# Optimization experiments

Measured on AMD Instinct MI355X. Metric: run time of the kernel, lower is better.

## Reference

```python
import jax, jax.numpy as jnp
import numpy as np

B, C, T, Fd = 4, 256, 64, 256
H = 8
HID = int(C * 2.0)
LN_EPS = 1e-5
L2_EPS = 1e-12


def _layernorm(x, g, b):
    mu = jnp.mean(x, axis=-1, keepdims=True)
    var = jnp.mean((x - mu) ** 2, axis=-1, keepdims=True)
    return (x - mu) * jax.lax.rsqrt(var + LN_EPS) * g + b


def _l2norm(x):
    n = jnp.sqrt(jnp.sum(x * x, axis=-1, keepdims=True))
    return x / jnp.maximum(n, L2_EPS)


def setup_inputs() -> dict:
    key = jax.random.key(0)
    ks = jax.random.split(key, 8)
    s = 0.02
    return {
        "x": jax.random.normal(ks[0], (B, C, T, Fd), dtype=jnp.float32),
        "norm1_g": jnp.ones((C,), jnp.float32),
        "norm1_b": jnp.zeros((C,), jnp.float32),
        "Wqkv": jax.random.normal(ks[1], (C, 3 * C), jnp.float32) * s,
        "dw_w": jax.random.normal(ks[2], (3 * C, 1, 3), jnp.float32) * s,  # depthwise conv1d kernel (O, I/g=1, K)
        "Wproj": jax.random.normal(ks[3], (C, C), jnp.float32) * s,
        "temperature": jnp.full((H, 1, 1), 0.5, jnp.float32),
        "norm2_g": jnp.ones((C,), jnp.float32),
        "norm2_b": jnp.zeros((C,), jnp.float32),
        "W1": jax.random.normal(ks[4], (C, HID), jnp.float32) * s,
        "b1": jnp.zeros((HID,), jnp.float32),
        "W2": jax.random.normal(ks[5], (HID, C), jnp.float32) * s,
        "b2": jnp.zeros((C,), jnp.float32),
    }


def reference(x, norm1_g, norm1_b, Wqkv, dw_w, Wproj, temperature,
              norm2_g, norm2_b, W1, b1, W2, b2):
    b, c, t, f = x.shape
    # axis='freq': (b c t f) -> ((b t) f c)
    xs = jnp.transpose(x, (0, 2, 3, 1)).reshape(b * t, f, c)

    xn = _layernorm(xs, norm1_g, norm1_b)
    qkv = xn @ Wqkv                                  # (bt, f, 3c)
    # depthwise conv1d along the sequence (freq) axis, kernel 3, pad 1
    qkv = jnp.transpose(qkv, (0, 2, 1))              # (bt, 3c, f)
    qkv = jax.lax.conv_general_dilated(
        qkv, dw_w, window_strides=(1,), padding=[(1, 1)],
        feature_group_count=3 * c,
        dimension_numbers=("NCH", "OIH", "NCH"))
    qkv = jnp.transpose(qkv, (0, 2, 1))              # (bt, f, 3c)

    q, k, v = jnp.split(qkv, 3, axis=-1)
    d = c // H
    def heads(z):  # (bt, s, c) -> (bt, h, s, d)
        return jnp.transpose(z.reshape(b * t, f, H, d), (0, 2, 1, 3))
    q, k, v = heads(q), heads(k), heads(v)

    q = _l2norm(q)
    k = _l2norm(k)
    attn = jnp.einsum("bhsd,bhtd->bhst", q, k) * temperature  # temp broadcasts (h,1,1)
    attn = jax.nn.softmax(attn, axis=-1)
    out = jnp.einsum("bhst,bhtd->bhsd", attn, v)
    out = jnp.transpose(out, (0, 2, 1, 3)).reshape(b * t, f, c)
    out = out @ Wproj
    out = out + xs

    h = _layernorm(out, norm2_g, norm2_b)
    h = jax.nn.gelu(h @ W1 + b1, approximate=False) @ W2 + b2
    out = out + h

    # ((b t) f c) -> (b c t f)
    out = out.reshape(b, t, f, c)
    return jnp.transpose(out, (0, 3, 1, 2))
```

## Files before the change

### kernel.cpp

```cpp
#include <hip/hip_runtime.h>
#include <math.h>

#define Bv 4
#define Cv 256
#define Tv 64
#define Fv 256
#define Hv 8
#define HIDv 512
#define Mv 65536
#define CTF (Cv * Tv * Fv)
#define TF (Tv * Fv)

typedef unsigned short u16;
typedef __attribute__((ext_vector_type(8))) short bfx8;
typedef __attribute__((ext_vector_type(4))) float f32x4;

__device__ __forceinline__ float bf2f(u16 u) {
  return __uint_as_float(((unsigned int)u) << 16);
}
__device__ __forceinline__ u16 f2bf(float f) {
  unsigned int x = __float_as_uint(f);
  unsigned int r = x + 0x7fffu + ((x >> 16) & 1u);
  return (u16)(r >> 16);
}

__launch_bounds__(256)
__global__ void transpose_w(const float* __restrict__ in, u16* __restrict__ out,
                            int K, int N) {
  __shared__ float t[32][33];
  const int n0 = blockIdx.x * 32, k0 = blockIdx.y * 32;
  const int c = threadIdx.x & 31, r = threadIdx.x >> 5;
#pragma unroll
  for (int i = 0; i < 4; ++i)
    t[r + 8 * i][c] = in[(size_t)(k0 + r + 8 * i) * N + n0 + c];
  __syncthreads();
#pragma unroll
  for (int i = 0; i < 4; ++i)
    out[(size_t)(n0 + r + 8 * i) * K + k0 + c] = f2bf(t[c][r + 8 * i]);
}

__launch_bounds__(256)
__global__ void ln1_kernel(const float* __restrict__ x, const float* __restrict__ g,
                           const float* __restrict__ bta, u16* __restrict__ xn) {
  __shared__ float tile[256][33];
  __shared__ float red1[8][32];
  __shared__ float red2[8][32];
  __shared__ float mu_s[32];
  __shared__ float rs_s[32];
  const int tid = threadIdx.x;
  const int blk = blockIdx.x;
  const int n = blk >> 3;
  const int f0 = (blk & 7) << 5;
  const int bb = n >> 6, tt = n & 63;
  const float* xb = x + (size_t)bb * CTF + (size_t)tt * Fv;
  const int fl = tid & 31, c0 = tid >> 5;
#pragma unroll
  for (int i = 0; i < 32; ++i) {
    int c = i * 8 + c0;
    tile[c][fl] = xb[(size_t)c * TF + f0 + fl];
  }
  __syncthreads();
  const int col = tid & 31, part = tid >> 5;
  float s = 0.f, s2 = 0.f;
#pragma unroll
  for (int i = 0; i < 32; ++i) {
    float v = tile[part * 32 + i][col];
    s += v; s2 += v * v;
  }
  red1[part][col] = s; red2[part][col] = s2;
  __syncthreads();
  if (tid < 32) {
    float S1 = 0.f, S2 = 0.f;
#pragma unroll
    for (int p = 0; p < 8; ++p) { S1 += red1[p][tid]; S2 += red2[p][tid]; }
    float m = S1 * (1.f / 256.f);
    float var = S2 * (1.f / 256.f) - m * m;
    mu_s[tid] = m;
    rs_s[tid] = rsqrtf(var + 1e-5f);
  }
  __syncthreads();
  const float gv = g[tid], bv = bta[tid];
  u16* ob = xn + ((size_t)n * 256 + f0) * 256 + tid;
#pragma unroll
  for (int fl2 = 0; fl2 < 32; ++fl2) {
    ob[(size_t)fl2 * 256] = f2bf((tile[tid][fl2] - mu_s[fl2]) * rs_s[fl2] * gv + bv);
  }
}

template <int K, int N, int EPI>
__launch_bounds__(256)
__global__ void gemm_mfma(const u16* __restrict__ A, const u16* __restrict__ Bt,
                          void* __restrict__ Cc, const float* __restrict__ aux0,
                          const u16* __restrict__ aux1) {
  constexpr int LDSTR = 88;
  __shared__ u16 As[128 * LDSTR];
  __shared__ u16 Bs[128 * LDSTR];
  const int tid = threadIdx.x;
  const int lane = tid & 63, wid = tid >> 6;
  const int m0 = blockIdx.y * 128, n0 = blockIdx.x * 128;
  const int wm = (wid & 1) * 64, wn = (wid >> 1) * 64;
  const int lm = lane & 15, quad = lane >> 4;

  const int srow = tid >> 3, sch = tid & 7;

  f32x4 acc[4][4] = {};
  for (int k0 = 0; k0 < K; k0 += 64) {
    bfx8 ar[4], br[4];
#pragma unroll
    for (int i = 0; i < 4; ++i) {
      const int row = srow + i * 32;
      ar[i] = *(const bfx8*)(A + (size_t)(m0 + row) * K + k0 + sch * 8);
      br[i] = *(const bfx8*)(Bt + (size_t)(n0 + row) * K + k0 + sch * 8);
    }
    __syncthreads();
#pragma unroll
    for (int i = 0; i < 4; ++i) {
      const int row = srow + i * 32;
      *(bfx8*)&As[row * LDSTR + sch * 8] = ar[i];
      *(bfx8*)&Bs[row * LDSTR + sch * 8] = br[i];
    }
    __syncthreads();
#pragma unroll
    for (int s = 0; s < 2; ++s) {
      bfx8 af[4], bf[4];
#pragma unroll
      for (int t = 0; t < 4; ++t) {
        af[t] = *(const bfx8*)&As[(wm + t * 16 + lm) * LDSTR + s * 32 + quad * 8];
        bf[t] = *(const bfx8*)&Bs[(wn + t * 16 + lm) * LDSTR + s * 32 + quad * 8];
      }
#pragma unroll
      for (int tm = 0; tm < 4; ++tm)
#pragma unroll
        for (int tn = 0; tn < 4; ++tn)
          acc[tm][tn] = __builtin_amdgcn_mfma_f32_16x16x32_bf16(af[tm], bf[tn], acc[tm][tn], 0, 0, 0);
    }
  }

  const int row_l = quad * 4;
  const int nn = m0 >> 8;
  const int bb = nn >> 6, tt = nn & 63;
  const int srow_base = (m0 & 255) + wm;
  float bcol[4];
  if constexpr (EPI == 2 || EPI == 3) {
#pragma unroll
    for (int tn = 0; tn < 4; ++tn) bcol[tn] = aux0[n0 + wn + tn * 16 + lm];
  }
#pragma unroll
  for (int tm = 0; tm < 4; ++tm) {
    const int grow0 = m0 + wm + tm * 16 + row_l;
    const int sr0 = srow_base + tm * 16 + row_l;
#pragma unroll
    for (int tn = 0; tn < 4; ++tn) {
      const int gcol = n0 + wn + tn * 16 + lm;
      if constexpr (EPI == 0) {
#pragma unroll
        for (int r = 0; r < 4; ++r)
          ((u16*)Cc)[(size_t)(grow0 + r) * N + gcol] = f2bf(acc[tm][tn][r]);
      } else if constexpr (EPI == 1) {
        const float4 xv = *(const float4*)(aux0 + (size_t)bb * CTF + (size_t)gcol * TF + tt * Fv + sr0);
        const float xr[4] = {xv.x, xv.y, xv.z, xv.w};
#pragma unroll
        for (int r = 0; r < 4; ++r)
          ((u16*)Cc)[(size_t)(grow0 + r) * N + gcol] = f2bf(acc[tm][tn][r] + xr[r]);
      } else if constexpr (EPI == 2) {
#pragma unroll
        for (int r = 0; r < 4; ++r) {
          float v = acc[tm][tn][r] + bcol[tn];
          float y = 0.79788456080286536f * (v + 0.044715f * v * v * v);
          float th = 1.f - 2.f / (__expf(2.f * y) + 1.f);
          ((u16*)Cc)[(size_t)(grow0 + r) * N + gcol] = f2bf(0.5f * v * (1.f + th));
        }
      } else {
        float4 o;
#pragma unroll
        for (int r = 0; r < 4; ++r) {
          float res = bf2f(aux1[(size_t)(grow0 + r) * 256 + gcol]);
          ((float*)&o)[r] = acc[tm][tn][r] + bcol[tn] + res;
        }
        *(float4*)((float*)Cc + (size_t)bb * CTF + (size_t)gcol * TF + tt * Fv + sr0) = o;
      }
    }
  }
}

__launch_bounds__(256)
__global__ void attn_kernel(const u16* __restrict__ qkv, const float* __restrict__ dw,
                            const float* __restrict__ temp, u16* __restrict__ attn_out) {
  __shared__ u16 Qs[256 * 40];
  __shared__ u16 Kc[64 * 40];
  __shared__ u16 Vtc[32 * 72];
  __shared__ u16 Pw[4 * 64 * 72];
  __shared__ float l_s[256];
  const int tid = threadIdx.x;
  const int lane = tid & 63, w = tid >> 6;
  const int l15 = lane & 15, quad = lane >> 4;
  const int n = blockIdx.x >> 3, h = blockIdx.x & 7;
  const int h32 = h * 32;
  const u16* base = qkv + (size_t)n * 256 * 768;
  const float th = temp[h];

  const int dg = tid & 3, d0 = dg * 8;
  const int rloc = tid >> 2;

  float wtsK[3][8], wtsV[3][8];
#pragma unroll
  for (int j = 0; j < 8; ++j) {
    const int chk = 256 + h32 + d0 + j;
    const int chv = 512 + h32 + d0 + j;
#pragma unroll
    for (int t = 0; t < 3; ++t) {
      wtsK[t][j] = dw[chk * 3 + t];
      wtsV[t][j] = dw[chv * 3 + t];
    }
  }

  {
    float wtsQ[3][8];
#pragma unroll
    for (int j = 0; j < 8; ++j)
#pragma unroll
      for (int t = 0; t < 3; ++t) wtsQ[t][j] = dw[(h32 + d0 + j) * 3 + t];
#pragma unroll
    for (int p = 0; p < 4; ++p) {
      const int row = p * 64 + rloc;
      const u16* src = base + (size_t)row * 768 + h32 + d0;
      float v[8];
      const bfx8 bmid = *(const bfx8*)src;
#pragma unroll
      for (int j = 0; j < 8; ++j) v[j] = wtsQ[1][j] * bf2f((u16)bmid[j]);
      if (row > 0) {
        const bfx8 bprv = *(const bfx8*)(src - 768);
#pragma unroll
        for (int j = 0; j < 8; ++j) v[j] += wtsQ[0][j] * bf2f((u16)bprv[j]);
      }
      if (row < 255) {
        const bfx8 bnxt = *(const bfx8*)(src + 768);
#pragma unroll
        for (int j = 0; j < 8; ++j) v[j] += wtsQ[2][j] * bf2f((u16)bnxt[j]);
      }
      float ssq = 0.f;
#pragma unroll
      for (int j = 0; j < 8; ++j) ssq += v[j] * v[j];
      ssq += __shfl_xor(ssq, 1);
      ssq += __shfl_xor(ssq, 2);
      const float inv = 1.f / fmaxf(sqrtf(ssq), 1e-12f);
      bfx8 qb;
#pragma unroll
      for (int j = 0; j < 8; ++j) qb[j] = (short)f2bf(v[j] * inv);
      *(bfx8*)&Qs[row * 40 + d0] = qb;
    }
  }
  __syncthreads();

  bfx8 bq[4];
#pragma unroll
  for (int ct = 0; ct < 4; ++ct)
    bq[ct] = *(const bfx8*)&Qs[(w * 64 + ct * 16 + l15) * 40 + quad * 8];

  u16* PwB = Pw + w * (64 * 72);
  const f32x4 zf = {0.f, 0.f, 0.f, 0.f};
  f32x4 acc[4][2] = {};
  float lsum[4] = {0.f, 0.f, 0.f, 0.f};

  for (int c = 0; c < 4; ++c) {
    {
      const int grow = c * 64 + rloc;
      const u16* srcK = base + (size_t)grow * 768 + 256 + h32 + d0;
      float v[8];
      const bfx8 bmid = *(const bfx8*)srcK;
#pragma unroll
      for (int j = 0; j < 8; ++j) v[j] = wtsK[1][j] * bf2f((u16)bmid[j]);
      if (grow > 0) {
        const bfx8 bprv = *(const bfx8*)(srcK - 768);
#pragma unroll
        for (int j = 0; j < 8; ++j) v[j] += wtsK[0][j] * bf2f((u16)bprv[j]);
      }
      if (grow < 255) {
        const bfx8 bnxt = *(const bfx8*)(srcK + 768);
#pragma unroll
        for (int j = 0; j < 8; ++j) v[j] += wtsK[2][j] * bf2f((u16)bnxt[j]);
      }
      float ssq = 0.f;
#pragma unroll
      for (int j = 0; j < 8; ++j) ssq += v[j] * v[j];
      ssq += __shfl_xor(ssq, 1);
      ssq += __shfl_xor(ssq, 2);
      const float inv = 1.f / fmaxf(sqrtf(ssq), 1e-12f);
      bfx8 kb;
#pragma unroll
      for (int j = 0; j < 8; ++j) kb[j] = (short)f2bf(v[j] * inv);
      *(bfx8*)&Kc[rloc * 40 + d0] = kb;

      const u16* srcV = base + (size_t)grow * 768 + 512 + h32 + d0;
      float vv[8];
      const bfx8 vmid = *(const bfx8*)srcV;
#pragma unroll
      for (int j = 0; j < 8; ++j) vv[j] = wtsV[1][j] * bf2f((u16)vmid[j]);
      if (grow > 0) {
        const bfx8 vprv = *(const bfx8*)(srcV - 768);
#pragma unroll
        for (int j = 0; j < 8; ++j) vv[j] += wtsV[0][j] * bf2f((u16)vprv[j]);
      }
      if (grow < 255) {
        const bfx8 vnxt = *(const bfx8*)(srcV + 768);
#pragma unroll
        for (int j = 0; j < 8; ++j) vv[j] += wtsV[2][j] * bf2f((u16)vnxt[j]);
      }
#pragma unroll
      for (int j = 0; j < 8; ++j) Vtc[(d0 + j) * 72 + rloc] = f2bf(vv[j]);
    }
    __syncthreads();

#pragma unroll
    for (int rt = 0; rt < 4; ++rt) {
      const bfx8 af = *(const bfx8*)&Kc[(rt * 16 + l15) * 40 + quad * 8];
#pragma unroll
      for (int ct = 0; ct < 4; ++ct) {
        f32x4 sc = __builtin_amdgcn_mfma_f32_16x16x32_bf16(af, bq[ct], zf, 0, 0, 0);
        float e0 = __expf(sc[0] * th);
        float e1 = __expf(sc[1] * th);
        float e2 = __expf(sc[2] * th);
        float e3 = __expf(sc[3] * th);
        lsum[ct] += (e0 + e1) + (e2 + e3);
        uint2 pk;
        pk.x = (unsigned int)f2bf(e0) | ((unsigned int)f2bf(e1) << 16);
        pk.y = (unsigned int)f2bf(e2) | ((unsigned int)f2bf(e3) << 16);
        *(uint2*)&PwB[(ct * 16 + l15) * 72 + rt * 16 + quad * 4] = pk;
      }
    }

#pragma unroll
    for (int ks = 0; ks < 2; ++ks) {
      const bfx8 bv0 = *(const bfx8*)&Vtc[l15 * 72 + ks * 32 + quad * 8];
      const bfx8 bv1 = *(const bfx8*)&Vtc[(16 + l15) * 72 + ks * 32 + quad * 8];
#pragma unroll
      for (int rt2 = 0; rt2 < 4; ++rt2) {
        const bfx8 ap = *(const bfx8*)&PwB[(rt2 * 16 + l15) * 72 + ks * 32 + quad * 8];
        acc[rt2][0] = __builtin_amdgcn_mfma_f32_16x16x32_bf16(ap, bv0, acc[rt2][0], 0, 0, 0);
        acc[rt2][1] = __builtin_amdgcn_mfma_f32_16x16x32_bf16(ap, bv1, acc[rt2][1], 0, 0, 0);
      }
    }
    __syncthreads();
  }

#pragma unroll
  for (int ct = 0; ct < 4; ++ct) {
    float L = lsum[ct];
    L += __shfl_xor(L, 16);
    L += __shfl_xor(L, 32);
    if (quad == 0) l_s[w * 64 + ct * 16 + l15] = L;
  }
  __syncthreads();

#pragma unroll
  for (int rt2 = 0; rt2 < 4; ++rt2) {
    const f32x4 l4 = *(const f32x4*)&l_s[w * 64 + rt2 * 16 + quad * 4];
    float rinv[4];
#pragma unroll
    for (int r = 0; r < 4; ++r) rinv[r] = 1.f / l4[r];
#pragma unroll
    for (int ct2 = 0; ct2 < 2; ++ct2) {
#pragma unroll
      for (int r = 0; r < 4; ++r) {
        const int qrow = w * 64 + rt2 * 16 + quad * 4 + r;
        attn_out[((size_t)n * 256 + qrow) * 256 + h32 + ct2 * 16 + l15] =
            f2bf(acc[rt2][ct2][r] * rinv[r]);
      }
    }
  }
}

__launch_bounds__(256)
__global__ void ln2_kernel(const u16* __restrict__ in, const float* __restrict__ g,
                           const float* __restrict__ bta, u16* __restrict__ out) {
  const int lane = threadIdx.x & 63;
  const size_t row = (size_t)blockIdx.x * 4 + (threadIdx.x >> 6);
  const ushort4 u = ((const ushort4*)(in + row * 256))[lane];
  const float vx = bf2f(u.x), vy = bf2f(u.y), vz = bf2f(u.z), vw = bf2f(u.w);
  float s = vx + vy + vz + vw;
  float s2 = vx * vx + vy * vy + vz * vz + vw * vw;
#pragma unroll
  for (int m = 32; m >= 1; m >>= 1) {
    s += __shfl_xor(s, m, 64);
    s2 += __shfl_xor(s2, m, 64);
  }
  const float mu = s * (1.f / 256.f);
  const float rs = rsqrtf(s2 * (1.f / 256.f) - mu * mu + 1e-5f);
  const float4 gv = ((const float4*)g)[lane];
  const float4 bv = ((const float4*)bta)[lane];
  ushort4 o;
  o.x = f2bf((vx - mu) * rs * gv.x + bv.x);
  o.y = f2bf((vy - mu) * rs * gv.y + bv.y);
  o.z = f2bf((vz - mu) * rs * gv.z + bv.z);
  o.w = f2bf((vw - mu) * rs * gv.w + bv.w);
  ((ushort4*)(out + row * 256))[lane] = o;
}

extern "C" void kernel_launch(void* const* d_in, const int* in_sizes, int n_in,
                              void* d_out, int out_size, void* d_ws, size_t ws_size,
                              hipStream_t stream) {
  const float* x     = (const float*)d_in[0];
  const float* n1g   = (const float*)d_in[1];
  const float* n1b   = (const float*)d_in[2];
  const float* Wqkv  = (const float*)d_in[3];
  const float* dw    = (const float*)d_in[4];
  const float* Wproj = (const float*)d_in[5];
  const float* temp  = (const float*)d_in[6];
  const float* n2g   = (const float*)d_in[7];
  const float* n2b   = (const float*)d_in[8];
  const float* W1    = (const float*)d_in[9];
  const float* b1    = (const float*)d_in[10];
  const float* W2    = (const float*)d_in[11];
  const float* b2    = (const float*)d_in[12];

  char* ws = (char*)d_ws;
  u16* xn       = (u16*)(ws);
  u16* qkv      = (u16*)(ws + (32ull << 20));
  u16* attn_out = xn;
  u16* out1     = (u16*)(ws + (32ull << 20));
  u16* xn2      = xn;
  u16* h1       = (u16*)(ws + (64ull << 20));
  u16* w2t      = xn;

  char* ob = (char*)d_out;
  u16* wqkvt  = (u16*)(ob);
  u16* wprojt = (u16*)(ob + (1ull << 20));
  u16* w1t    = (u16*)(ob + 1572864ull);

  transpose_w<<<dim3(24, 8), 256, 0, stream>>>(Wqkv, wqkvt, 256, 768);
  transpose_w<<<dim3(8, 8), 256, 0, stream>>>(Wproj, wprojt, 256, 256);
  transpose_w<<<dim3(16, 8), 256, 0, stream>>>(W1, w1t, 256, 512);

  ln1_kernel<<<2048, 256, 0, stream>>>(x, n1g, n1b, xn);
  gemm_mfma<256, 768, 0><<<dim3(6, 512), 256, 0, stream>>>(xn, wqkvt, qkv, nullptr, nullptr);
  attn_kernel<<<2048, 256, 0, stream>>>(qkv, dw, temp, attn_out);
  gemm_mfma<256, 256, 1><<<dim3(2, 512), 256, 0, stream>>>(attn_out, wprojt, out1, x, nullptr);
  ln2_kernel<<<16384, 256, 0, stream>>>(out1, n2g, n2b, xn2);
  gemm_mfma<256, 512, 2><<<dim3(4, 512), 256, 0, stream>>>(xn2, W1 ? w1t : w1t, h1, b1, nullptr);
  transpose_w<<<dim3(8, 16), 256, 0, stream>>>(W2, w2t, 512, 256);
  gemm_mfma<512, 256, 3><<<dim3(2, 512), 256, 0, stream>>>(h1, w2t, d_out, b2, out1);
}
```

Baseline: 417.6 us.

## Load GEMM tiles directly to LDS with XOR-swizzled layout

The GEMM tile staging now uses global_load_lds so global data goes straight into shared memory without passing through registers. The padded LDS rows are replaced by an unpadded 64-element stride with an XOR swizzle on 16-byte chunks, which is meant to avoid bank conflicts on the MFMA fragment reads. A trailing barrier is added to protect the single buffer. This frees registers and VGPR staging work, but there is still no double buffering, so load latency is not overlapped with compute.

```diff
diff --git a/kernel.cpp b/kernel.cpp
--- a/kernel.cpp
+++ b/kernel.cpp
@@ -22,6 +22,12 @@
   unsigned int x = __float_as_uint(f);
   unsigned int r = x + 0x7fffu + ((x >> 16) & 1u);
   return (u16)(r >> 16);
+}
+
+typedef const void __attribute__((address_space(1)))* gvp;
+typedef void __attribute__((address_space(3)))* lvp;
+__device__ __forceinline__ void async_cp16(const u16* g, u16* l) {
+  __builtin_amdgcn_global_load_lds((gvp)g, (lvp)l, 16, 0, 0);
 }
 
 __launch_bounds__(256)
@@ -92,32 +98,26 @@
 __global__ void gemm_mfma(const u16* __restrict__ A, const u16* __restrict__ Bt,
                           void* __restrict__ Cc, const float* __restrict__ aux0,
                           const u16* __restrict__ aux1) {
-  constexpr int LDSTR = 88;
-  __shared__ u16 As[128 * LDSTR];
-  __shared__ u16 Bs[128 * LDSTR];
+  __shared__ u16 As[128 * 64];
+  __shared__ u16 Bs[128 * 64];
   const int tid = threadIdx.x;
   const int lane = tid & 63, wid = tid >> 6;
   const int m0 = blockIdx.y * 128, n0 = blockIdx.x * 128;
   const int wm = (wid & 1) * 64, wn = (wid >> 1) * 64;
   const int lm = lane & 15, quad = lane >> 4;
 
-  const int srow = tid >> 3, sch = tid & 7;
+  const int lrow = lane >> 3;
+  const int lchunk = (lane & 7) ^ lrow;
 
   f32x4 acc[4][4] = {};
   for (int k0 = 0; k0 < K; k0 += 64) {
-    bfx8 ar[4], br[4];
 #pragma unroll
     for (int i = 0; i < 4; ++i) {
-      const int row = srow + i * 32;
-      ar[i] = *(const bfx8*)(A + (size_t)(m0 + row) * K + k0 + sch * 8);
-      br[i] = *(const bfx8*)(Bt + (size_t)(n0 + row) * K + k0 + sch * 8);
-    }
-    __syncthreads();
-#pragma unroll
-    for (int i = 0; i < 4; ++i) {
-      const int row = srow + i * 32;
-      *(bfx8*)&As[row * LDSTR + sch * 8] = ar[i];
-      *(bfx8*)&Bs[row * LDSTR + sch * 8] = br[i];
+      const int rbase = wid * 32 + i * 8;
+      async_cp16(A + (size_t)(m0 + rbase + lrow) * K + k0 + lchunk * 8,
+                 As + rbase * 64);
+      async_cp16(Bt + (size_t)(n0 + rbase + lrow) * K + k0 + lchunk * 8,
+                 Bs + rbase * 64);
     }
     __syncthreads();
 #pragma unroll
@@ -125,8 +125,9 @@
       bfx8 af[4], bf[4];
 #pragma unroll
       for (int t = 0; t < 4; ++t) {
-        af[t] = *(const bfx8*)&As[(wm + t * 16 + lm) * LDSTR + s * 32 + quad * 8];
-        bf[t] = *(const bfx8*)&Bs[(wn + t * 16 + lm) * LDSTR + s * 32 + quad * 8];
+        const int slot = ((s * 4 + quad) ^ (lm & 7)) * 8;
+        af[t] = *(const bfx8*)&As[(wm + t * 16 + lm) * 64 + slot];
+        bf[t] = *(const bfx8*)&Bs[(wn + t * 16 + lm) * 64 + slot];
       }
 #pragma unroll
       for (int tm = 0; tm < 4; ++tm)
@@ -134,6 +135,7 @@
         for (int tn = 0; tn < 4; ++tn)
           acc[tm][tn] = __builtin_amdgcn_mfma_f32_16x16x32_bf16(af[tm], bf[tn], acc[tm][tn], 0, 0, 0);
     }
+    __syncthreads();
   }
 
   const int row_l = quad * 4;
@@ -436,7 +438,7 @@
   attn_kernel<<<2048, 256, 0, stream>>>(qkv, dw, temp, attn_out);
   gemm_mfma<256, 256, 1><<<dim3(2, 512), 256, 0, stream>>>(attn_out, wprojt, out1, x, nullptr);
   ln2_kernel<<<16384, 256, 0, stream>>>(out1, n2g, n2b, xn2);
-  gemm_mfma<256, 512, 2><<<dim3(4, 512), 256, 0, stream>>>(xn2, W1 ? w1t : w1t, h1, b1, nullptr);
+  gemm_mfma<256, 512, 2><<<dim3(4, 512), 256, 0, stream>>>(xn2, w1t, h1, b1, nullptr);
   transpose_w<<<dim3(8, 16), 256, 0, stream>>>(W2, w2t, 512, 256);
   gemm_mfma<512, 256, 3><<<dim3(2, 512), 256, 0, stream>>>(h1, w2t, d_out, b2, out1);
 }
```

New measurement: 421.5 us. Within noise of the previous version (+0.9%).
